# Kernel optimization log

Measured on AMD Instinct MI355X. Metric: run time of the kernel, lower is better.

Reference implementation:

```python
import jax, jax.numpy as jnp
import numpy as np

NUM_AREAS = 4
NUM_TICKS = 4
AREA_N = 2048          # neurons per area
N = NUM_AREAS * AREA_N # total neurons = 8192
D_IN = 1024
N_CLASSES = 1024
BATCH = 512
THRESHOLD = 0.05


def setup_inputs() -> dict:
    key = jax.random.key(0)
    ks = jax.random.split(key, 9)
    x = jax.random.normal(ks[0], (BATCH, D_IN), jnp.float32)
    Rw = jax.random.normal(ks[1], (NUM_AREAS, AREA_N, D_IN), jnp.float32) * 0.02
    rb = jax.random.normal(ks[2], (NUM_AREAS, AREA_N), jnp.float32) * 0.02
    W_blocks = jax.random.normal(ks[3], (NUM_AREAS, NUM_AREAS, AREA_N, AREA_N), jnp.float32) * 0.02
    # bias only on diagonal blocks (in_area == out_area), else zeros, as in torch code
    b_full = jax.random.normal(ks[4], (NUM_AREAS, AREA_N), jnp.float32) * 0.02
    b_blocks = jnp.zeros((NUM_AREAS, NUM_AREAS, AREA_N), jnp.float32)
    b_blocks = b_blocks.at[jnp.arange(NUM_AREAS), jnp.arange(NUM_AREAS)].set(b_full)
    # mask init: 0.5 on diagonal blocks, 0.05 off-diagonal
    eye = jnp.eye(NUM_AREAS, dtype=jnp.float32)
    mask = (0.05 + 0.45 * eye)[:, :, None, None] * jnp.ones((NUM_AREAS, NUM_AREAS, AREA_N, AREA_N), jnp.float32)
    Ow = jax.random.normal(ks[5], (N_CLASSES, N), jnp.float32) * 0.02
    Ob = jax.random.normal(ks[6], (N_CLASSES,), jnp.float32) * 0.02
    # KMeans-like neuron partition: random permutation split into equal areas
    area_idx = jax.random.permutation(ks[7], N).reshape(NUM_AREAS, AREA_N).astype(jnp.int64)
    return {"x": x, "Rw": Rw, "rb": rb, "W_blocks": W_blocks, "b_blocks": b_blocks,
            "mask": mask, "Ow": Ow, "Ob": Ob, "area_idx": area_idx}


def reference(x, Rw, rb, W_blocks, b_blocks, mask, Ow, Ob, area_idx):
    # Initial per-area encoding: Z[a] = tanh(x @ Rw[a].T + rb[a]) -> [A, B, n]
    Z = jnp.tanh(jnp.einsum('bd,and->abn', x, Rw) + rb[:, None, :])
    history = [Z]
    # Effective masked weights (clamp mask to [0,1])
    Weff = W_blocks * jnp.clip(mask, 0.0, 1.0)  # [A_out, A_in, n_out, n_in]
    for _ in range(NUM_TICKS):
        # data-dependent skip: connection fires only if mean|Z_in| > threshold
        gate = (jnp.mean(jnp.abs(Z), axis=(1, 2)) > THRESHOLD).astype(Z.dtype)  # [A_in]
        Zg = Z * gate[:, None, None]
        Z_next = jnp.einsum('ibm,oinm->obn', Zg, Weff)
        Z_next = Z_next + jnp.einsum('i,oin->on', gate, b_blocks)[:, None, :]
        Z = jnp.tanh(Z_next)
        history.append(Z)
    B = x.shape[0]
    # Scatter per-area activations back to flat neuron order
    Zperm = jnp.transpose(Z, (1, 0, 2)).reshape(B, N)  # columns ordered as area_idx.reshape(-1)
    Z_flat = jnp.zeros((B, N), x.dtype).at[:, area_idx.reshape(-1)].set(Zperm)
    logits = Z_flat @ Ow.T + Ob
    return logits, jnp.stack(history)  # history: [T+1, A, B, n]
```

## Files before the change

kernel.cpp:

```cpp
#include <hip/hip_runtime.h>
#include <stdint.h>

typedef unsigned short u16;
typedef float floatx4 __attribute__((ext_vector_type(4)));
typedef __bf16 bf16x8 __attribute__((ext_vector_type(8)));
typedef float f32x4v __attribute__((ext_vector_type(4)));
typedef unsigned u32x4v __attribute__((ext_vector_type(4)));

#define NUM_AREAS 4
#define AN 2048
#define NTOT 8192
#define BATCH 512
#define DIN 1024
#define NCLS 1024
#define THRESHOLD 0.05f
#define BAN (BATCH * AN)

__device__ __forceinline__ size_t zpk(int a, int b, int n) {
    return ((((size_t)a * 2 + (b >> 8)) * 64 + (n >> 5)) << 13) | ((b & 255) << 5) | (n & 31);
}


__device__ __forceinline__ u16 f2bf(float f) {
    union { float f; unsigned u; } v; v.f = f;
    unsigned r = v.u + 0x7fffu + ((v.u >> 16) & 1u);
    return (u16)(r >> 16);
}

__device__ __forceinline__ void load_lds16(const u16* g, u16* l) {
    __builtin_amdgcn_global_load_lds((const __attribute__((address_space(1))) void*)g,
                                     (__attribute__((address_space(3))) void*)l,
                                     16, 0, 0);
}

__device__ __forceinline__ void gemm_db(const u16* __restrict__ A, int lda,
                                        const u16* __restrict__ Bm, int ldb,
                                        int klen, u16* sA, u16* sB,
                                        floatx4 acc[4][4]) {
    const int tid = threadIdx.x;
    const int t8 = tid * 8;
    const int lane = tid & 63;
    const int quad = lane >> 4;
    const int l15 = lane & 15;
    const int qs8 = (quad ^ ((l15 >> 1) & 3)) * 8;
    const int wm = ((tid >> 7) & 1) * 64;
    const int wn = ((tid >> 6) & 1) * 64;
    const int r0 = t8 >> 5;
    const int kks = (((tid & 3) ^ ((tid >> 3) & 3)) << 3);
    const int nst = klen >> 5;

    auto stage = [&](int buf, int k0) {
        const int bo = buf << 12;
        load_lds16(A + (size_t)r0 * lda + (k0 + kks), sA + bo + t8);
        load_lds16(Bm + (size_t)r0 * ldb + (k0 + kks), sB + bo + t8);
        load_lds16(A + (size_t)(r0 + 64) * lda + (k0 + kks), sA + bo + 2048 + t8);
        load_lds16(Bm + (size_t)(r0 + 64) * ldb + (k0 + kks), sB + bo + 2048 + t8);
    };

    stage(0, 0);
    __syncthreads();
    int buf = 0;
    for (int t = 0; t < nst; ++t) {
        const int bo = buf << 12;
        bf16x8 av[4], bv[4];
#pragma unroll
        for (int i = 0; i < 4; ++i)
            av[i] = *(const bf16x8*)(sA + bo + (wm + i * 16 + l15) * 32 + qs8);
#pragma unroll
        for (int i = 0; i < 4; ++i)
            bv[i] = *(const bf16x8*)(sB + bo + (wn + i * 16 + l15) * 32 + qs8);
        if (t + 1 < nst) stage(buf ^ 1, (t + 1) << 5);
#pragma unroll
        for (int mt = 0; mt < 4; ++mt)
#pragma unroll
            for (int nt = 0; nt < 4; ++nt)
                acc[mt][nt] = __builtin_amdgcn_mfma_f32_16x16x32_bf16(av[mt], bv[nt], acc[mt][nt], 0, 0, 0);
        __syncthreads();
        buf ^= 1;
    }
}

__global__ void k_init(const float* __restrict__ Ob, float* __restrict__ out,
                       float* __restrict__ gacc) {
    const int i = blockIdx.x * 256 + threadIdx.x;
    if (i < BATCH * NCLS) out[i] = Ob[i & (NCLS - 1)];
    if (i < 32) gacc[i] = 0.f;
}

__global__ void k_cvt(const float* __restrict__ src, u16* __restrict__ dst, int n8) {
    const int i = blockIdx.x * 256 + threadIdx.x;
    if (i >= n8) return;
    const float4 x0 = ((const float4*)src)[2 * i];
    const float4 x1 = ((const float4*)src)[2 * i + 1];
    uint4 o;
    o.x = (unsigned)f2bf(x0.x) | ((unsigned)f2bf(x0.y) << 16);
    o.y = (unsigned)f2bf(x0.z) | ((unsigned)f2bf(x0.w) << 16);
    o.z = (unsigned)f2bf(x1.x) | ((unsigned)f2bf(x1.y) << 16);
    o.w = (unsigned)f2bf(x1.z) | ((unsigned)f2bf(x1.w) << 16);
    ((uint4*)dst)[i] = o;
}

#define CLM(m) fminf(fmaxf((m), 0.f), 1.f)
#define PKW(wa, ma, wb, mb) ((unsigned)f2bf((wa) * CLM(ma)) | ((unsigned)f2bf((wb) * CLM(mb)) << 16))

__global__ void k_weffp(const float* __restrict__ W, const float* __restrict__ mask,
                        u16* __restrict__ dst) {
    const int ktg = blockIdx.x, nb = blockIdx.y, o4i = blockIdx.z;
    const int t = threadIdx.x;
    u16* dt = dst + (((size_t)o4i * 8 + nb) * 64 + (size_t)ktg * 4) * 8192;
    const float* Wb = W + ((size_t)o4i * 2048 + nb * 256) * 2048;
    const float* Mb = mask + ((size_t)o4i * 2048 + nb * 256) * 2048;
    const int kk = (t & 3) * 8;
    const int rb = t >> 2;
#pragma unroll
    for (int s = 0; s < 4; ++s) {
        const int k0 = (ktg * 4 + s) * 32 + kk;
#pragma unroll
        for (int v = 0; v < 4; ++v) {
            const int r = v * 64 + rb;
            const float4* wp = (const float4*)(Wb + (size_t)r * 2048 + k0);
            const float4* mp = (const float4*)(Mb + (size_t)r * 2048 + k0);
            const float4 w0 = wp[0], w1 = wp[1];
            const float4 m0 = mp[0], m1 = mp[1];
            uint4 ov;
            ov.x = PKW(w0.x, m0.x, w0.y, m0.y);
            ov.y = PKW(w0.z, m0.z, w0.w, m0.w);
            ov.z = PKW(w1.x, m1.x, w1.y, m1.y);
            ov.w = PKW(w1.z, m1.z, w1.w, m1.w);
            *(uint4*)(dt + (size_t)s * 8192 + (size_t)v * 2048 + t * 8) = ov;
        }
    }
}

__global__ void k_enc(const u16* __restrict__ xbf, const u16* __restrict__ rwbf,
                      const float* __restrict__ rb, float* __restrict__ hist0,
                      u16* __restrict__ z0, float* __restrict__ gacc) {
    __shared__ __align__(16) u16 smemA[8192];
    __shared__ __align__(16) u16 smemB[8192];
    __shared__ float red[4];
    floatx4 acc[4][4] = {};
    const int mb = blockIdx.y, nb = blockIdx.x;
    gemm_db(xbf + (size_t)mb * 128 * DIN, DIN,
            rwbf + (size_t)nb * 128 * DIN, DIN, DIN, smemA, smemB, acc);
    const int tid = threadIdx.x, lane = tid & 63, quad = lane >> 4, l15 = lane & 15;
    const int wm = ((tid >> 7) & 1) * 64, wn = ((tid >> 6) & 1) * 64;
    const int cbase = nb * 128;
    const int area = cbase >> 11;
    float asum = 0.f;
#pragma unroll
    for (int nt = 0; nt < 4; ++nt) {
        const int col = cbase + wn + nt * 16 + l15;
        const int n = col & (AN - 1);
        const float bias = rb[col];
#pragma unroll
        for (int mt = 0; mt < 4; ++mt) {
#pragma unroll
            for (int r = 0; r < 4; ++r) {
                const int row = mb * 128 + wm + mt * 16 + quad * 4 + r;
                const float z = tanhf(acc[mt][nt][r] + bias);
                asum += fabsf(z);
                hist0[(size_t)area * BAN + (size_t)row * AN + n] = z;
                z0[zpk(area, row, n)] = f2bf(z);
            }
        }
    }
    for (int off = 32; off > 0; off >>= 1) asum += __shfl_down(asum, off, 64);
    if (lane == 0) red[tid >> 6] = asum;
    __syncthreads();
    if (tid == 0) atomicAdd(&gacc[area], red[0] + red[1] + red[2] + red[3]);
}

__global__ __launch_bounds__(512, 2)
void k_tick_mm(const u16* __restrict__ zprev, const u16* __restrict__ weff,
               const float* __restrict__ gin, float* __restrict__ zacc) {
    __shared__ __align__(16) u16 sA[3][8192];
    __shared__ __align__(16) u16 sB[3][8192];
    const int nb = blockIdx.x, mb = blockIdx.y, i = blockIdx.z;
    const float thr = THRESHOLD * (float)BAN;
    if (!(gin[i] > thr)) return;

    const int o = nb >> 3;
    const int nb8 = nb & 7;
    const int nbase = nb8 * 256;
    const int tid = threadIdx.x;
    const int lane = tid & 63, quad = lane >> 4, l15 = lane & 15;
    const int qs8 = (quad ^ ((l15 >> 1) & 3)) * 8;
    const int w = tid >> 6;
    const int wm = (w >> 2) * 128;
    const int wn = (w & 3) * 64;

    const int swt = (tid ^ ((tid >> 3) & 3)) * 8;
    const u16* Ap = zprev + ((size_t)(i * 2 + mb) * 64) * 8192 + swt;
    const u16* Bp = weff + ((size_t)((o * 4 + i) * 8 + nb8) * 64) * 8192 + swt;
    u16* dA = &sA[0][tid * 8];
    u16* dB = &sB[0][tid * 8];

    auto stage = [&](int slot, int kt) {
        const size_t go = (size_t)kt * 8192;
        const int so = slot * 8192;
        load_lds16(Ap + go, dA + so);
        load_lds16(Ap + go + 4096, dA + so + 4096);
        load_lds16(Bp + go, dB + so);
        load_lds16(Bp + go + 4096, dB + so + 4096);
    };

    floatx4 acc[8][4] = {};

    stage(0, 0);
    stage(1, 1);
    asm volatile("s_waitcnt vmcnt(4)" ::: "memory");
    __builtin_amdgcn_s_barrier();

    const int NKT = AN / 32;
    for (int kt = 0; kt < NKT; ++kt) {
        if (kt + 2 < NKT) stage((kt + 2) % 3, kt + 2);
        const int sl = kt % 3;
        bf16x8 av[8], bv[4];
#pragma unroll
        for (int mt = 0; mt < 8; ++mt)
            av[mt] = *(const bf16x8*)(&sA[sl][(wm + mt * 16 + l15) * 32 + qs8]);
#pragma unroll
        for (int nt = 0; nt < 4; ++nt)
            bv[nt] = *(const bf16x8*)(&sB[sl][(wn + nt * 16 + l15) * 32 + qs8]);
        __builtin_amdgcn_s_setprio(1);
#pragma unroll
        for (int mt = 0; mt < 8; ++mt)
#pragma unroll
            for (int nt = 0; nt < 4; ++nt)
                acc[mt][nt] = __builtin_amdgcn_mfma_f32_16x16x32_bf16(av[mt], bv[nt], acc[mt][nt], 0, 0, 0);
        __builtin_amdgcn_s_setprio(0);
        if (kt < NKT - 2) {
            asm volatile("s_waitcnt vmcnt(4)" ::: "memory");
        } else {
            asm volatile("s_waitcnt vmcnt(0)" ::: "memory");
        }
        __builtin_amdgcn_s_barrier();
    }

    float* __restrict__ dst = zacc + ((size_t)i * 4 + o) * BAN;
#pragma unroll
    for (int mt = 0; mt < 8; ++mt) {
#pragma unroll
        for (int nt = 0; nt < 4; ++nt) {
            const int n = nbase + wn + nt * 16 + l15;
#pragma unroll
            for (int r = 0; r < 4; ++r) {
                const int row = mb * 256 + wm + mt * 16 + quad * 4 + r;
                dst[(size_t)row * AN + n] = acc[mt][nt][r];
            }
        }
    }
}

__global__ void k_tick_ep(const float* __restrict__ zacc, const float* __restrict__ bblk,
                          const float* __restrict__ gin, float* __restrict__ hist,
                          u16* __restrict__ zcur, float* __restrict__ gout) {
    __shared__ float red[4];
    const int tid = threadIdx.x;
    const int t8 = (blockIdx.x * 256 + tid) * 8;
    const int o = t8 >> 20;
    const int n = t8 & (AN - 1);
    const int io = t8 & (BAN - 1);
    const int b = io >> 11;
    const float thr = THRESHOLD * (float)BAN;
    float s[8] = {0.f, 0.f, 0.f, 0.f, 0.f, 0.f, 0.f, 0.f};
#pragma unroll
    for (int i = 0; i < 4; ++i) {
        if (!(gin[i] > thr)) continue;
        const float4* p = (const float4*)(zacc + ((size_t)i * 4 + o) * BAN + io);
        const float4 x0 = p[0], x1 = p[1];
        const float4* bb = (const float4*)(bblk + (size_t)(o * 4 + i) * AN + n);
        const float4 b0 = bb[0], b1 = bb[1];
        s[0] += x0.x + b0.x; s[1] += x0.y + b0.y; s[2] += x0.z + b0.z; s[3] += x0.w + b0.w;
        s[4] += x1.x + b1.x; s[5] += x1.y + b1.y; s[6] += x1.z + b1.z; s[7] += x1.w + b1.w;
    }
    float4 h0, h1;
    uint4 zb;
    const float z0 = tanhf(s[0]), z1 = tanhf(s[1]), z2 = tanhf(s[2]), z3 = tanhf(s[3]);
    const float z4 = tanhf(s[4]), z5 = tanhf(s[5]), z6 = tanhf(s[6]), z7 = tanhf(s[7]);
    float asum = fabsf(z0) + fabsf(z1) + fabsf(z2) + fabsf(z3)
               + fabsf(z4) + fabsf(z5) + fabsf(z6) + fabsf(z7);
    h0.x = z0; h0.y = z1; h0.z = z2; h0.w = z3;
    h1.x = z4; h1.y = z5; h1.z = z6; h1.w = z7;
    zb.x = (unsigned)f2bf(z0) | ((unsigned)f2bf(z1) << 16);
    zb.y = (unsigned)f2bf(z2) | ((unsigned)f2bf(z3) << 16);
    zb.z = (unsigned)f2bf(z4) | ((unsigned)f2bf(z5) << 16);
    zb.w = (unsigned)f2bf(z6) | ((unsigned)f2bf(z7) << 16);
    ((float4*)(hist + t8))[0] = h0;
    ((float4*)(hist + t8))[1] = h1;
    *((uint4*)(zcur + zpk(o, b, n))) = zb;
    for (int off = 32; off > 0; off >>= 1) asum += __shfl_down(asum, off, 64);
    if ((tid & 63) == 0) red[tid >> 6] = asum;
    __syncthreads();
    if (tid == 0) atomicAdd(&gout[o], red[0] + red[1] + red[2] + red[3]);
}

__global__ void k_scatter(const u16* __restrict__ z4, const int* __restrict__ aidx,
                          u16* __restrict__ zflat) {
    const int i = blockIdx.x * 256 + threadIdx.x;
    const int a = i >> 20;
    const int rest = i & (BAN - 1);
    const int tile = rest >> 13;
    const int within = rest & 8191;
    const int b = ((tile >> 6) << 8) | (within >> 5);
    const int n = ((tile & 63) << 5) | (within & 31);
    const int j = aidx[a * AN + n];
    zflat[(size_t)b * NTOT + j] = z4[i];
}

__global__ void k_out(const u16* __restrict__ zflat, const u16* __restrict__ owbf,
                      float* __restrict__ out) {
    __shared__ __align__(16) u16 smemA[8192];
    __shared__ __align__(16) u16 smemB[8192];
    floatx4 acc[4][4] = {};
    const int nb = blockIdx.x, mb = blockIdx.y, ks = blockIdx.z;
    gemm_db(zflat + (size_t)mb * 128 * NTOT + ks * 1024, NTOT,
            owbf + (size_t)nb * 128 * NTOT + ks * 1024, NTOT, 1024,
            smemA, smemB, acc);
    const int tid = threadIdx.x, lane = tid & 63, quad = lane >> 4, l15 = lane & 15;
    const int wm = ((tid >> 7) & 1) * 64, wn = ((tid >> 6) & 1) * 64;
#pragma unroll
    for (int mt = 0; mt < 4; ++mt)
#pragma unroll
        for (int nt = 0; nt < 4; ++nt)
#pragma unroll
            for (int r = 0; r < 4; ++r) {
                const int row = mb * 128 + wm + mt * 16 + quad * 4 + r;
                const int col = nb * 128 + wn + nt * 16 + l15;
                atomicAdd(&out[(size_t)row * NCLS + col], acc[mt][nt][r]);
            }
}

extern "C" void kernel_launch(void* const* d_in, const int* in_sizes, int n_in,
                              void* d_out, int out_size, void* d_ws, size_t ws_size,
                              hipStream_t stream) {
    (void)in_sizes; (void)n_in; (void)out_size; (void)ws_size;
    const float* x    = (const float*)d_in[0];
    const float* Rw   = (const float*)d_in[1];
    const float* rb   = (const float*)d_in[2];
    const float* Wb   = (const float*)d_in[3];
    const float* bblk = (const float*)d_in[4];
    const float* mask = (const float*)d_in[5];
    const float* Ow   = (const float*)d_in[6];
    const float* Ob   = (const float*)d_in[7];
    const int*   aidx = (const int*)d_in[8];

    float* out  = (float*)d_out;
    float* hist = out + (size_t)BATCH * NCLS;

    char* ws = (char*)d_ws;
    size_t off = 0;
    auto alloc = [&](size_t bytes) -> char* {
        char* p = ws + off;
        off += (bytes + 255) & ~(size_t)255;
        return p;
    };
    u16* weffbf = (u16*)alloc((size_t)16 * AN * AN * 2);
    float* zacc = (float*)alloc((size_t)16 * BAN * 4);
    u16* rwbf  = (u16*)zacc;
    u16* owbf  = (u16*)((char*)zacc + ((size_t)16 << 20));
    u16* zflat = (u16*)((char*)zacc + ((size_t)32 << 20));
    u16* xbf    = (u16*)alloc((size_t)BATCH * DIN * 2);
    u16* zb0    = (u16*)alloc((size_t)NUM_AREAS * BAN * 2);
    u16* zb1    = (u16*)alloc((size_t)NUM_AREAS * BAN * 2);
    float* gacc = (float*)alloc(32 * 4);
    u16* zb[2]  = { zb0, zb1 };

    k_init<<<(BATCH * NCLS + 255) / 256, 256, 0, stream>>>(Ob, out, gacc);
    k_cvt<<<(BATCH * DIN / 8) / 256, 256, 0, stream>>>(x, xbf, BATCH * DIN / 8);
    k_cvt<<<(NTOT * DIN / 8) / 256, 256, 0, stream>>>(Rw, rwbf, NTOT * DIN / 8);
    k_weffp<<<dim3(16, 8, 16), 256, 0, stream>>>(Wb, mask, weffbf);

    dim3 g1(64, 4);
    k_enc<<<g1, 256, 0, stream>>>(xbf, rwbf, rb, hist, zb[0], gacc);
    dim3 gmm(32, 2, 4);
    for (int t = 1; t <= 4; ++t) {
        k_tick_mm<<<gmm, 512, 0, stream>>>(zb[(t + 1) & 1], weffbf,
                                           gacc + (t - 1) * 4, zacc);
        k_tick_ep<<<2048, 256, 0, stream>>>(zacc, bblk, gacc + (t - 1) * 4,
                                            hist + (size_t)t * NUM_AREAS * BAN,
                                            zb[t & 1], gacc + t * 4);
    }
    k_cvt<<<(NCLS * NTOT / 8) / 256, 256, 0, stream>>>(Ow, owbf, NCLS * NTOT / 8);
    k_scatter<<<(NUM_AREAS * BAN) / 256, 256, 0, stream>>>(zb[0], aidx, zflat);
    k_out<<<dim3(8, 4, 8), 256, 0, stream>>>(zflat, owbf, out);
}
```

Measured before the change: 1.122 ms.

## Repack Z and Weff into 128x64 XOR-swizzled tiles with K=64 double-buffered tick GEMM

```diff
diff --git a/kernel.cpp b/kernel.cpp
--- a/kernel.cpp
+++ b/kernel.cpp
@@ -16,10 +16,11 @@
 #define THRESHOLD 0.05f
 #define BAN (BATCH * AN)
 
-__device__ __forceinline__ size_t zpk(int a, int b, int n) {
-    return ((((size_t)a * 2 + (b >> 8)) * 64 + (n >> 5)) << 13) | ((b & 255) << 5) | (n & 31);
-}
-
+__device__ __forceinline__ size_t zpk2(int a, int b, int n) {
+    const int rowblk = b >> 7, r = b & 127, kt = n >> 6, k = n & 63;
+    const int kc = ((k >> 3) ^ (r & 7));
+    return ((((size_t)a * 4 + rowblk) * 32 + kt) << 13) + r * 64 + (kc << 3) + (k & 7);
+}
 
 __device__ __forceinline__ u16 f2bf(float f) {
     union { float f; unsigned u; } v; v.f = f;
@@ -105,30 +106,27 @@
 
 __global__ void k_weffp(const float* __restrict__ W, const float* __restrict__ mask,
                         u16* __restrict__ dst) {
-    const int ktg = blockIdx.x, nb = blockIdx.y, o4i = blockIdx.z;
+    const int rsub = blockIdx.x, nblk = blockIdx.y, o4i = blockIdx.z;
     const int t = threadIdx.x;
-    u16* dt = dst + (((size_t)o4i * 8 + nb) * 64 + (size_t)ktg * 4) * 8192;
-    const float* Wb = W + ((size_t)o4i * 2048 + nb * 256) * 2048;
-    const float* Mb = mask + ((size_t)o4i * 2048 + nb * 256) * 2048;
-    const int kk = (t & 3) * 8;
-    const int rb = t >> 2;
-#pragma unroll
-    for (int s = 0; s < 4; ++s) {
-        const int k0 = (ktg * 4 + s) * 32 + kk;
-#pragma unroll
-        for (int v = 0; v < 4; ++v) {
-            const int r = v * 64 + rb;
-            const float4* wp = (const float4*)(Wb + (size_t)r * 2048 + k0);
-            const float4* mp = (const float4*)(Mb + (size_t)r * 2048 + k0);
-            const float4 w0 = wp[0], w1 = wp[1];
-            const float4 m0 = mp[0], m1 = mp[1];
-            uint4 ov;
-            ov.x = PKW(w0.x, m0.x, w0.y, m0.y);
-            ov.y = PKW(w0.z, m0.z, w0.w, m0.w);
-            ov.z = PKW(w1.x, m1.x, w1.y, m1.y);
-            ov.w = PKW(w1.z, m1.z, w1.w, m1.w);
-            *(uint4*)(dt + (size_t)s * 8192 + (size_t)v * 2048 + t * 8) = ov;
-        }
+    const int gr0 = nblk * 128 + rsub * 32;
+    const float* Wb = W + ((size_t)o4i * 2048 + gr0) * 2048;
+    const float* Mb = mask + ((size_t)o4i * 2048 + gr0) * 2048;
+    u16* dbase = dst + (((size_t)o4i * 16 + nblk) * 32) * 8192;
+    const int kt = t >> 3;
+    const int kc = t & 7;
+    for (int r = 0; r < 32; ++r) {
+        const int rr = rsub * 32 + r;
+        const float4* wp = (const float4*)(Wb + (size_t)r * 2048 + t * 8);
+        const float4* mp = (const float4*)(Mb + (size_t)r * 2048 + t * 8);
+        const float4 w0 = wp[0], w1 = wp[1];
+        const float4 m0 = mp[0], m1 = mp[1];
+        uint4 ov;
+        ov.x = PKW(w0.x, m0.x, w0.y, m0.y);
+        ov.y = PKW(w0.z, m0.z, w0.w, m0.w);
+        ov.z = PKW(w1.x, m1.x, w1.y, m1.y);
+        ov.w = PKW(w1.z, m1.z, w1.w, m1.w);
+        const int kcs = kc ^ (rr & 7);
+        *(uint4*)(dbase + (size_t)kt * 8192 + rr * 64 + kcs * 8) = ov;
     }
 }
 
@@ -160,7 +158,7 @@
                 const float z = tanhf(acc[mt][nt][r] + bias);
                 asum += fabsf(z);
                 hist0[(size_t)area * BAN + (size_t)row * AN + n] = z;
-                z0[zpk(area, row, n)] = f2bf(z);
+                z0[zpk2(area, row, n)] = f2bf(z);
             }
         }
     }
@@ -173,79 +171,94 @@
 __global__ __launch_bounds__(512, 2)
 void k_tick_mm(const u16* __restrict__ zprev, const u16* __restrict__ weff,
                const float* __restrict__ gin, float* __restrict__ zacc) {
-    __shared__ __align__(16) u16 sA[3][8192];
-    __shared__ __align__(16) u16 sB[3][8192];
-    const int nb = blockIdx.x, mb = blockIdx.y, i = blockIdx.z;
+    __shared__ __align__(16) u16 sA[2][2][8192];
+    __shared__ __align__(16) u16 sB[2][2][8192];
+    const int id = blockIdx.x;
+    const int mb = id >> 7;
+    const int panel = id & 127;
+    const int i = panel >> 5;
+    const int nb = panel & 31;
     const float thr = THRESHOLD * (float)BAN;
     if (!(gin[i] > thr)) return;
-
-    const int o = nb >> 3;
-    const int nb8 = nb & 7;
+    const int o = nb >> 3, nb8 = nb & 7;
+    const int tid = threadIdx.x, lane = tid & 63, quad = lane >> 4, l15 = lane & 15;
+    const int w = tid >> 6, wr = w >> 2, wc = w & 3;
+    const int cs0 = ((quad ^ (l15 & 7)) << 3);
+    const int cs1 = (((4 | quad) ^ (l15 & 7)) << 3);
+    const u16* Ab = zprev + (((size_t)i * 4 + mb * 2) * 32) * 8192 + tid * 8;
+    const u16* Bb = weff + ((((size_t)(o * 4 + i)) * 16 + nb8 * 2) * 32) * 8192 + tid * 8;
+
+    auto stageA = [&](int buf, int h, int kt) {
+        const u16* s = Ab + ((size_t)h * 32 + kt) * 8192;
+        u16* d = &sA[buf][h][tid * 8];
+        load_lds16(s, d);
+        load_lds16(s + 4096, d + 4096);
+    };
+    auto stageB = [&](int buf, int h, int kt) {
+        const u16* s = Bb + ((size_t)h * 32 + kt) * 8192;
+        u16* d = &sB[buf][h][tid * 8];
+        load_lds16(s, d);
+        load_lds16(s + 4096, d + 4096);
+    };
+
+    floatx4 acc[8][4] = {};
+    bf16x8 bv[4][2];
+    const int hb = wc >> 1;
+    const int cb = (wc & 1) << 6;
+
+    stageA(0, 0, 0); stageA(0, 1, 0); stageB(0, 0, 0); stageB(0, 1, 0);
+
+    for (int kt = 0; kt < 32; ++kt) {
+        const int buf = kt & 1;
+        asm volatile("s_waitcnt vmcnt(0)" ::: "memory");
+        __builtin_amdgcn_s_barrier();
+        const u16* A0 = &sA[buf][wr][0];
+        const u16* B0 = &sB[buf][hb][0];
+#pragma unroll
+        for (int p = 0; p < 4; ++p) {
+            const int r0 = (p * 2) * 16 + l15;
+            const bf16x8 av0k0 = *(const bf16x8*)(A0 + r0 * 64 + cs0);
+            const bf16x8 av0k1 = *(const bf16x8*)(A0 + r0 * 64 + cs1);
+            const bf16x8 av1k0 = *(const bf16x8*)(A0 + (r0 + 16) * 64 + cs0);
+            const bf16x8 av1k1 = *(const bf16x8*)(A0 + (r0 + 16) * 64 + cs1);
+            if (p == 0) {
+#pragma unroll
+                for (int nt = 0; nt < 4; ++nt) {
+                    const int rb2 = cb + nt * 16 + l15;
+                    bv[nt][0] = *(const bf16x8*)(B0 + rb2 * 64 + cs0);
+                    bv[nt][1] = *(const bf16x8*)(B0 + rb2 * 64 + cs1);
+                }
+            }
+            if (kt + 1 < 32) {
+                if (p == 0) { stageB(buf ^ 1, 0, kt + 1); stageB(buf ^ 1, 1, kt + 1); }
+                else if (p == 1) { stageA(buf ^ 1, 0, kt + 1); stageA(buf ^ 1, 1, kt + 1); }
+            }
+            __builtin_amdgcn_s_barrier();
+            asm volatile("s_waitcnt lgkmcnt(0)" ::: "memory");
+            __builtin_amdgcn_sched_barrier(0);
+            __builtin_amdgcn_s_setprio(1);
+#pragma unroll
+            for (int nt = 0; nt < 4; ++nt) {
+                acc[2 * p][nt] = __builtin_amdgcn_mfma_f32_16x16x32_bf16(av0k0, bv[nt][0], acc[2 * p][nt], 0, 0, 0);
+                acc[2 * p][nt] = __builtin_amdgcn_mfma_f32_16x16x32_bf16(av0k1, bv[nt][1], acc[2 * p][nt], 0, 0, 0);
+                acc[2 * p + 1][nt] = __builtin_amdgcn_mfma_f32_16x16x32_bf16(av1k0, bv[nt][0], acc[2 * p + 1][nt], 0, 0, 0);
+                acc[2 * p + 1][nt] = __builtin_amdgcn_mfma_f32_16x16x32_bf16(av1k1, bv[nt][1], acc[2 * p + 1][nt], 0, 0, 0);
+            }
+            __builtin_amdgcn_s_setprio(0);
+            __builtin_amdgcn_s_barrier();
+        }
+    }
+
+    float* __restrict__ dst = zacc + ((size_t)i * 4 + o) * BAN;
     const int nbase = nb8 * 256;
-    const int tid = threadIdx.x;
-    const int lane = tid & 63, quad = lane >> 4, l15 = lane & 15;
-    const int qs8 = (quad ^ ((l15 >> 1) & 3)) * 8;
-    const int w = tid >> 6;
-    const int wm = (w >> 2) * 128;
-    const int wn = (w & 3) * 64;
-
-    const int swt = (tid ^ ((tid >> 3) & 3)) * 8;
-    const u16* Ap = zprev + ((size_t)(i * 2 + mb) * 64) * 8192 + swt;
-    const u16* Bp = weff + ((size_t)((o * 4 + i) * 8 + nb8) * 64) * 8192 + swt;
-    u16* dA = &sA[0][tid * 8];
-    u16* dB = &sB[0][tid * 8];
-
-    auto stage = [&](int slot, int kt) {
-        const size_t go = (size_t)kt * 8192;
-        const int so = slot * 8192;
-        load_lds16(Ap + go, dA + so);
-        load_lds16(Ap + go + 4096, dA + so + 4096);
-        load_lds16(Bp + go, dB + so);
-        load_lds16(Bp + go + 4096, dB + so + 4096);
-    };
-
-    floatx4 acc[8][4] = {};
-
-    stage(0, 0);
-    stage(1, 1);
-    asm volatile("s_waitcnt vmcnt(4)" ::: "memory");
-    __builtin_amdgcn_s_barrier();
-
-    const int NKT = AN / 32;
-    for (int kt = 0; kt < NKT; ++kt) {
-        if (kt + 2 < NKT) stage((kt + 2) % 3, kt + 2);
-        const int sl = kt % 3;
-        bf16x8 av[8], bv[4];
-#pragma unroll
-        for (int mt = 0; mt < 8; ++mt)
-            av[mt] = *(const bf16x8*)(&sA[sl][(wm + mt * 16 + l15) * 32 + qs8]);
-#pragma unroll
-        for (int nt = 0; nt < 4; ++nt)
-            bv[nt] = *(const bf16x8*)(&sB[sl][(wn + nt * 16 + l15) * 32 + qs8]);
-        __builtin_amdgcn_s_setprio(1);
-#pragma unroll
-        for (int mt = 0; mt < 8; ++mt)
-#pragma unroll
-            for (int nt = 0; nt < 4; ++nt)
-                acc[mt][nt] = __builtin_amdgcn_mfma_f32_16x16x32_bf16(av[mt], bv[nt], acc[mt][nt], 0, 0, 0);
-        __builtin_amdgcn_s_setprio(0);
-        if (kt < NKT - 2) {
-            asm volatile("s_waitcnt vmcnt(4)" ::: "memory");
-        } else {
-            asm volatile("s_waitcnt vmcnt(0)" ::: "memory");
-        }
-        __builtin_amdgcn_s_barrier();
-    }
-
-    float* __restrict__ dst = zacc + ((size_t)i * 4 + o) * BAN;
 #pragma unroll
     for (int mt = 0; mt < 8; ++mt) {
 #pragma unroll
         for (int nt = 0; nt < 4; ++nt) {
-            const int n = nbase + wn + nt * 16 + l15;
+            const int n = nbase + wc * 64 + nt * 16 + l15;
 #pragma unroll
             for (int r = 0; r < 4; ++r) {
-                const int row = mb * 256 + wm + mt * 16 + quad * 4 + r;
+                const int row = mb * 256 + wr * 128 + mt * 16 + quad * 4 + r;
                 dst[(size_t)row * AN + n] = acc[mt][nt][r];
             }
         }
@@ -288,7 +301,7 @@
     zb.w = (unsigned)f2bf(z6) | ((unsigned)f2bf(z7) << 16);
     ((float4*)(hist + t8))[0] = h0;
     ((float4*)(hist + t8))[1] = h1;
-    *((uint4*)(zcur + zpk(o, b, n))) = zb;
+    *((uint4*)(zcur + zpk2(o, b, n))) = zb;
     for (int off = 32; off > 0; off >>= 1) asum += __shfl_down(asum, off, 64);
     if ((tid & 63) == 0) red[tid >> 6] = asum;
     __syncthreads();
@@ -299,13 +312,9 @@
                           u16* __restrict__ zflat) {
     const int i = blockIdx.x * 256 + threadIdx.x;
     const int a = i >> 20;
-    const int rest = i & (BAN - 1);
-    const int tile = rest >> 13;
-    const int within = rest & 8191;
-    const int b = ((tile >> 6) << 8) | (within >> 5);
-    const int n = ((tile & 63) << 5) | (within & 31);
-    const int j = aidx[a * AN + n];
-    zflat[(size_t)b * NTOT + j] = z4[i];
+    const int b = (i >> 11) & (BATCH - 1);
+    const int n = i & (AN - 1);
+    zflat[(size_t)b * NTOT + aidx[a * AN + n]] = z4[zpk2(a, b, n)];
 }
 
 __global__ void k_out(const u16* __restrict__ zflat, const u16* __restrict__ owbf,
@@ -369,13 +378,12 @@
     k_init<<<(BATCH * NCLS + 255) / 256, 256, 0, stream>>>(Ob, out, gacc);
     k_cvt<<<(BATCH * DIN / 8) / 256, 256, 0, stream>>>(x, xbf, BATCH * DIN / 8);
     k_cvt<<<(NTOT * DIN / 8) / 256, 256, 0, stream>>>(Rw, rwbf, NTOT * DIN / 8);
-    k_weffp<<<dim3(16, 8, 16), 256, 0, stream>>>(Wb, mask, weffbf);
+    k_weffp<<<dim3(4, 16, 16), 256, 0, stream>>>(Wb, mask, weffbf);
 
     dim3 g1(64, 4);
     k_enc<<<g1, 256, 0, stream>>>(xbf, rwbf, rb, hist, zb[0], gacc);
-    dim3 gmm(32, 2, 4);
     for (int t = 1; t <= 4; ++t) {
-        k_tick_mm<<<gmm, 512, 0, stream>>>(zb[(t + 1) & 1], weffbf,
+        k_tick_mm<<<256, 512, 0, stream>>>(zb[(t + 1) & 1], weffbf,
                                            gacc + (t - 1) * 4, zacc);
         k_tick_ep<<<2048, 256, 0, stream>>>(zacc, bblk, gacc + (t - 1) * 4,
                                             hist + (size_t)t * NUM_AREAS * BAN,
```

After: 1.083 ms. 1.04x faster.
